# Kernel tuning notes

Measured on AMD Instinct MI355X. Metric: run time of the kernel, lower is better.

The kernel has to match this reference:

```python
import jax, jax.numpy as jnp
import numpy as np

D_MODEL = 1024
N_HEADS = 16
N_GROUPS = 4
HEAD_DIM = D_MODEL // N_HEADS
HPG = N_HEADS // N_GROUPS


def setup_inputs() -> dict:
    key = jax.random.key(0)
    ks = jax.random.split(key, 9)
    B, T = 4, 2048
    s = 1.0 / np.sqrt(D_MODEL)
    kv_dim = N_GROUPS * HEAD_DIM
    return {
        "x": jax.random.normal(ks[0], (B, T, D_MODEL), dtype=jnp.float32),
        "Wq": jax.random.normal(ks[1], (D_MODEL, D_MODEL), dtype=jnp.float32) * s,
        "bq": jnp.zeros((D_MODEL,), dtype=jnp.float32),
        "Wk": jax.random.normal(ks[2], (D_MODEL, kv_dim), dtype=jnp.float32) * s,
        "bk": jnp.zeros((kv_dim,), dtype=jnp.float32),
        "Wv": jax.random.normal(ks[3], (D_MODEL, kv_dim), dtype=jnp.float32) * s,
        "bv": jnp.zeros((kv_dim,), dtype=jnp.float32),
        "Wo": jax.random.normal(ks[4], (D_MODEL, D_MODEL), dtype=jnp.float32) * s,
        "bo": jnp.zeros((D_MODEL,), dtype=jnp.float32),
    }


def reference(x, Wq, bq, Wk, bk, Wv, bv, Wo, bo):
    B, T, _ = x.shape
    q = x @ Wq + bq                                  # [B,T,D]
    k = x @ Wk + bk                                  # [B,T,G*hd]
    v = x @ Wv + bv
    q = q.reshape(B, T, N_HEADS, HEAD_DIM).transpose(0, 2, 1, 3)   # [B,H,T,hd]
    k = k.reshape(B, T, N_GROUPS, HEAD_DIM).transpose(0, 2, 1, 3)  # [B,G,T,hd]
    v = v.reshape(B, T, N_GROUPS, HEAD_DIM).transpose(0, 2, 1, 3)
    # repeat_interleave KV groups to match Q heads
    k = jnp.repeat(k, HPG, axis=1)                   # [B,H,T,hd]
    v = jnp.repeat(v, HPG, axis=1)
    scale = 1.0 / np.sqrt(HEAD_DIM).astype(np.float32)
    scores = jnp.einsum('bhqd,bhkd->bhqk', q, k) * scale  # [B,H,T,T]
    attn = jax.nn.softmax(scores, axis=-1)
    out = jnp.einsum('bhqk,bhkd->bhqd', attn, v)     # [B,H,T,hd]
    out = out.transpose(0, 2, 1, 3).reshape(B, T, D_MODEL)
    return out @ Wo + bo
```

## Files before the change

### kernel.cpp

```cpp
#include <hip/hip_runtime.h>
#include <stdint.h>

#define D_MODEL 1024
#define T_SEQ   2048
#define BATCH   4
#define NH      16
#define NG      4
#define HD      64

#define QSCALE 0.18033688611f

typedef short bf16x8 __attribute__((ext_vector_type(8)));
typedef float f32x4  __attribute__((ext_vector_type(4)));

__device__ __forceinline__ f32x4 mfma16(bf16x8 a, bf16x8 b, f32x4 c) {
    return __builtin_amdgcn_mfma_f32_16x16x32_bf16(a, b, c, 0, 0, 0);
}

__device__ __forceinline__ unsigned short f2bf(float f) {
    __bf16 h = (__bf16)f;
    return __builtin_bit_cast(unsigned short, h);
}

__global__ __launch_bounds__(256) void prep(
        const float* __restrict__ x,  unsigned short* __restrict__ xb,
        const float* __restrict__ Wq, unsigned short* __restrict__ Wqt,
        const float* __restrict__ Wk, unsigned short* __restrict__ Wkt,
        const float* __restrict__ Wv, unsigned short* __restrict__ Wvt,
        const float* __restrict__ Wo, unsigned short* __restrict__ Wot) {
    __shared__ unsigned short sh[32][33];
    int bid = blockIdx.x;
    if (bid < 8192) {
        int i = (bid * 256 + threadIdx.x) * 4;
        float4 v = *reinterpret_cast<const float4*>(x + i);
        ushort4 o;
        o.x = f2bf(v.x); o.y = f2bf(v.y); o.z = f2bf(v.z); o.w = f2bf(v.w);
        *reinterpret_cast<ushort4*>(xb + i) = o;
        return;
    }
    bid -= 8192;
    const float* src; unsigned short* dst; int N, nbx;
    if (bid < 1024)      { src = Wq; dst = Wqt; N = 1024; nbx = 32; }
    else if (bid < 1280) { bid -= 1024; src = Wk; dst = Wkt; N = 256;  nbx = 8; }
    else if (bid < 1536) { bid -= 1280; src = Wv; dst = Wvt; N = 256;  nbx = 8; }
    else                 { bid -= 1536; src = Wo; dst = Wot; N = 1024; nbx = 32; }
    const int K = 1024;
    int n0 = (bid % nbx) * 32, k0 = (bid / nbx) * 32;
    int tx = threadIdx.x & 31, ty = threadIdx.x >> 5;
#pragma unroll
    for (int j = 0; j < 4; j++) {
        int k = ty + 8 * j;
        sh[k][tx] = f2bf(src[(size_t)(k0 + k) * N + n0 + tx]);
    }
    __syncthreads();
#pragma unroll
    for (int j = 0; j < 4; j++) {
        int n = ty + 8 * j;
        dst[(size_t)(n0 + n) * K + k0 + tx] = sh[tx][n];
    }
}

template <int MODE>
__global__ __launch_bounds__(256) void gemm128(
        const unsigned short* __restrict__ A,
        const unsigned short* __restrict__ Bt,
        const float* __restrict__ b0, const float* __restrict__ b1,
        const float* __restrict__ b2,
        void* __restrict__ Cq, void* __restrict__ Ck, void* __restrict__ Cv,
        int K) {
    __shared__ unsigned short As[128 * 64];
    __shared__ unsigned short Bs[128 * 64];

    int tid  = threadIdx.x;
    int lane = tid & 63, w = tid >> 6;
    int wr = w >> 1, wc = w & 1;

    int nx  = gridDim.x;
    int lin = blockIdx.y * nx + blockIdx.x;
    int cpx = (nx * gridDim.y) >> 3;
    int nb  = (lin & 7) * cpx + (lin >> 3);
    int m0 = (nb / nx) * 128, n0 = (nb % nx) * 128;

    int lr = lane & 15, kg = lane >> 4;

    f32x4 acc[4][4] = {};

    const unsigned short* Ab = A  + (size_t)m0 * K;
    const unsigned short* Bb = Bt + (size_t)n0 * K;

    size_t soff[4];
    unsigned short* adst[4];
    unsigned short* bdst[4];
#pragma unroll
    for (int i = 0; i < 4; i++) {
        int ci  = i * 256 + tid;
        int row = ci >> 3, ch = ci & 7;
        int csrc = ch ^ (row & 7);
        soff[i] = (size_t)row * K + csrc * 8;
        adst[i] = As + (size_t)(i * 256 + w * 64) * 8;
        bdst[i] = Bs + (size_t)(i * 256 + w * 64) * 8;
    }

    for (int kt = 0; kt < K; kt += 64) {
#pragma unroll
        for (int i = 0; i < 4; i++) {
            __builtin_amdgcn_global_load_lds(
                (const __attribute__((address_space(1))) void*)(Ab + soff[i] + kt),
                (__attribute__((address_space(3))) void*)adst[i], 16, 0, 0);
            __builtin_amdgcn_global_load_lds(
                (const __attribute__((address_space(1))) void*)(Bb + soff[i] + kt),
                (__attribute__((address_space(3))) void*)bdst[i], 16, 0, 0);
        }
        __syncthreads();

        bf16x8 af[4][2], bf[4][2];
#pragma unroll
        for (int mt = 0; mt < 4; mt++) {
            int row = wr * 64 + mt * 16 + lr;
#pragma unroll
            for (int ks = 0; ks < 2; ks++) {
                int ch = (kg + ks * 4) ^ (row & 7);
                af[mt][ks] = *reinterpret_cast<const bf16x8*>(&As[row * 64 + ch * 8]);
            }
        }
#pragma unroll
        for (int nt = 0; nt < 4; nt++) {
            int row = wc * 64 + nt * 16 + lr;
#pragma unroll
            for (int ks = 0; ks < 2; ks++) {
                int ch = (kg + ks * 4) ^ (row & 7);
                bf[nt][ks] = *reinterpret_cast<const bf16x8*>(&Bs[row * 64 + ch * 8]);
            }
        }

#pragma unroll
        for (int ks = 0; ks < 2; ks++)
#pragma unroll
            for (int mt = 0; mt < 4; mt++)
#pragma unroll
                for (int nt = 0; nt < 4; nt++)
                    acc[mt][nt] = mfma16(af[mt][ks], bf[nt][ks], acc[mt][nt]);

        __syncthreads();
    }

    int rbase = kg * 4;
#pragma unroll
    for (int nt = 0; nt < 4; nt++) {
        int col = n0 + wc * 64 + nt * 16 + lr;
        float bias;
        if (MODE == 1)            bias = b0[col];
        else if (col < 1024)      bias = b0[col];
        else if (col < 1280)      bias = b1[col - 1024];
        else                      bias = b2[col - 1280];
#pragma unroll
        for (int mt = 0; mt < 4; mt++) {
#pragma unroll
            for (int r = 0; r < 4; r++) {
                int row = m0 + wr * 64 + mt * 16 + rbase + r;
                float v = acc[mt][nt][r] + bias;
                if (MODE == 1) {
                    ((float*)Cq)[(size_t)row * 1024 + col] = v;
                } else if (col < 1024) {
                    ((unsigned short*)Cq)[(size_t)row * 1024 + col] = f2bf(v * QSCALE);
                } else if (col < 1280) {
                    int cc = col - 1024, g = cc >> 6, d = cc & 63;
                    int b = row >> 11, t = row & 2047;
                    ((unsigned short*)Ck)[(((size_t)(b * NG + g)) * T_SEQ + t) * HD + d] = f2bf(v);
                } else {
                    int cc = col - 1280, g = cc >> 6, d = cc & 63;
                    int b = row >> 11, t = row & 2047;
                    ((unsigned short*)Cv)[(((size_t)(b * NG + g)) * HD + d) * T_SEQ + t] = f2bf(v);
                }
            }
        }
    }
}

__global__ __launch_bounds__(256) void attn_fwd(
        const unsigned short* __restrict__ Q,
        const unsigned short* __restrict__ Kt,
        const unsigned short* __restrict__ Vt,
        unsigned short* __restrict__ O) {
    int tid  = threadIdx.x;
    int lane = tid & 63;
    int w    = tid >> 6;
    int qt = blockIdx.x, h = blockIdx.y, b = blockIdx.z;
    int g = h >> 2;
    int lr  = lane & 15;
    int grp = lane >> 4;
    int ko  = grp * 8;
    int q0  = qt * 128 + w * 32;

    __shared__ unsigned short Kl[2][64 * 64];
    __shared__ unsigned short Vl[2][64 * 64];

    const unsigned short* Kp = Kt + ((size_t)(b * NG + g)) * T_SEQ * HD;
    const unsigned short* Vp = Vt + ((size_t)(b * NG + g)) * HD * T_SEQ;

    bf16x8 qf[2][2];
#pragma unroll
    for (int qi = 0; qi < 2; qi++) {
        const unsigned short* Qp =
            Q + ((size_t)(b * T_SEQ + q0 + qi * 16 + lr)) * D_MODEL + h * HD;
        qf[qi][0] = *reinterpret_cast<const bf16x8*>(Qp + ko);
        qf[qi][1] = *reinterpret_cast<const bf16x8*>(Qp + 32 + ko);
    }

    f32x4 oacc[2][4] = {};
    f32x4 den[2] = {};
    bf16x8 ones;
#pragma unroll
    for (int j = 0; j < 8; j++) ones[j] = (short)0x3F80;

    int loff[4][2];
#pragma unroll
    for (int c = 0; c < 4; c++) {
        int row = c * 16 + lr;
#pragma unroll
        for (int s = 0; s < 2; s++)
            loff[c][s] = row * 64 + (((s * 4 + grp) ^ (row & 7)) * 8);
    }

    const unsigned short* gkb[2];
    const unsigned short* gvb[2];
    unsigned short* lkd[2];
#pragma unroll
    for (int i = 0; i < 2; i++) {
        int ci  = i * 256 + tid;
        int row = ci >> 3, ch = ci & 7;
        int csrc = ch ^ (row & 7);
        int kp = 32 * (row >> 5) + 4 * ((row >> 4) & 1)
               + 8 * ((row >> 2) & 3) + (row & 3);
        gkb[i] = Kp + (size_t)kp * HD + csrc * 8;
        gvb[i] = Vp + (size_t)row * T_SEQ + csrc * 8;
        lkd[i] = (unsigned short*)((size_t)(i * 256 + w * 64) * 8);
    }

    auto STAGE = [&](int buf, int j0) {
#pragma unroll
        for (int i = 0; i < 2; i++) {
            size_t ldoff = (size_t)lkd[i];
            __builtin_amdgcn_global_load_lds(
                (const __attribute__((address_space(1))) void*)(gkb[i] + ((size_t)j0 << 6)),
                (__attribute__((address_space(3))) void*)(&Kl[buf][0] + ldoff), 16, 0, 0);
            __builtin_amdgcn_global_load_lds(
                (const __attribute__((address_space(1))) void*)(gvb[i] + j0),
                (__attribute__((address_space(3))) void*)(&Vl[buf][0] + ldoff), 16, 0, 0);
        }
    };

    auto do_tile = [&](int cur, int jt) {
        if (jt + 1 < T_SEQ / 64) STAGE(cur ^ 1, (jt + 1) * 64);

        const unsigned short* kb = &Kl[cur][0];
        const unsigned short* vb = &Vl[cur][0];

        bf16x8 kf[4][2], vf[4][2];
#pragma unroll
        for (int t = 0; t < 4; t++)
#pragma unroll
            for (int ks = 0; ks < 2; ks++)
                kf[t][ks] = *reinterpret_cast<const bf16x8*>(kb + loff[t][ks]);
#pragma unroll
        for (int dt = 0; dt < 4; dt++)
#pragma unroll
            for (int kh = 0; kh < 2; kh++)
                vf[dt][kh] = *reinterpret_cast<const bf16x8*>(vb + loff[dt][kh]);

#pragma unroll
        for (int qi = 0; qi < 2; qi++) {
            f32x4 s[4];
            __builtin_amdgcn_s_setprio(1);
#pragma unroll
            for (int t = 0; t < 4; t++) {
                f32x4 a = {};
                a = mfma16(kf[t][0], qf[qi][0], a);
                a = mfma16(kf[t][1], qf[qi][1], a);
                s[t] = a;
            }
            __builtin_amdgcn_s_setprio(0);

            float p[4][4];
#pragma unroll
            for (int t = 0; t < 4; t++)
#pragma unroll
                for (int r = 0; r < 4; r++)
                    asm("v_exp_f32 %0, %1" : "=v"(p[t][r]) : "v"(s[t][r]));

            bf16x8 pf0, pf1;
#pragma unroll
            for (int j = 0; j < 4; j++) {
                pf0[j]     = (short)f2bf(p[0][j]);
                pf0[j + 4] = (short)f2bf(p[1][j]);
                pf1[j]     = (short)f2bf(p[2][j]);
                pf1[j + 4] = (short)f2bf(p[3][j]);
            }

            __builtin_amdgcn_s_setprio(1);
#pragma unroll
            for (int dt = 0; dt < 4; dt++) {
                oacc[qi][dt] = mfma16(vf[dt][0], pf0, oacc[qi][dt]);
                oacc[qi][dt] = mfma16(vf[dt][1], pf1, oacc[qi][dt]);
            }
            den[qi] = mfma16(ones, pf0, den[qi]);
            den[qi] = mfma16(ones, pf1, den[qi]);
            __builtin_amdgcn_s_setprio(0);
        }

        asm volatile("s_waitcnt vmcnt(0)" ::: "memory");
        __syncthreads();
    };

    STAGE(0, 0);
    asm volatile("s_waitcnt vmcnt(0)" ::: "memory");
    __syncthreads();

    for (int jt = 0; jt < T_SEQ / 64; jt += 2) {
        do_tile(0, jt);
        do_tile(1, jt + 1);
    }

#pragma unroll
    for (int qi = 0; qi < 2; qi++) {
        float rinv = 1.0f / den[qi][0];
        size_t rowbase = ((size_t)(b * T_SEQ + q0 + qi * 16 + lr)) * D_MODEL + h * HD;
#pragma unroll
        for (int dt = 0; dt < 4; dt++) {
            ushort4 o;
#pragma unroll
            for (int r = 0; r < 4; r++)
                ((unsigned short*)&o)[r] = f2bf(oacc[qi][dt][r] * rinv);
            *reinterpret_cast<ushort4*>(&O[rowbase + dt * 16 + 4 * grp]) = o;
        }
    }
}

extern "C" void kernel_launch(void* const* d_in, const int* in_sizes, int n_in,
                              void* d_out, int out_size, void* d_ws, size_t ws_size,
                              hipStream_t stream) {
    const float* x  = (const float*)d_in[0];
    const float* Wq = (const float*)d_in[1];
    const float* bq = (const float*)d_in[2];
    const float* Wk = (const float*)d_in[3];
    const float* bk = (const float*)d_in[4];
    const float* Wv = (const float*)d_in[5];
    const float* bv = (const float*)d_in[6];
    const float* Wo = (const float*)d_in[7];
    const float* bo = (const float*)d_in[8];

    char* ws = (char*)d_ws;
    unsigned short* xb  = (unsigned short*)(ws);
    unsigned short* Wqt = (unsigned short*)(ws + 16777216);
    unsigned short* Wkt = (unsigned short*)(ws + 18874368);
    unsigned short* Wvt = (unsigned short*)(ws + 19398656);
    unsigned short* Wot = (unsigned short*)(ws + 19922944);
    unsigned short* Qb  = (unsigned short*)(ws + 22020096);
    unsigned short* Kb  = (unsigned short*)(ws + 38797312);
    unsigned short* Vtb = (unsigned short*)(ws + 42991616);

    prep<<<dim3(8192 + 2560), 256, 0, stream>>>(
        x, xb, Wq, Wqt, Wk, Wkt, Wv, Wvt, Wo, Wot);

    gemm128<0><<<dim3(12, 64), 256, 0, stream>>>(
        xb, Wqt, bq, bk, bv, Qb, Kb, Vtb, 1024);

    attn_fwd<<<dim3(T_SEQ / 128, NH, BATCH), 256, 0, stream>>>(Qb, Kb, Vtb, xb);

    gemm128<1><<<dim3(8, 64), 256, 0, stream>>>(
        xb, Wot, bo, nullptr, nullptr, d_out, nullptr, nullptr, 1024);
}
```

Baseline: 162.4 us.

## Triple-buffer K/V tiles in attention with two-ahead prefetch and partial vmcnt waits

Moves the attention kernel's K/V staging from double to triple buffering in LDS, so loads are issued two tiles ahead. Each step now waits only until the older tile's loads have completed (vmcnt(4)) and uses a raw s_barrier, so global_load_lds transfers can stay in flight across the barrier. This costs 50% more LDS per block, which may reduce occupancy, and depends on exact vmcnt accounting for correctness.

```diff
diff --git a/kernel.cpp b/kernel.cpp
--- a/kernel.cpp
+++ b/kernel.cpp
@@ -192,8 +192,8 @@
     int ko  = grp * 8;
     int q0  = qt * 128 + w * 32;
 
-    __shared__ unsigned short Kl[2][64 * 64];
-    __shared__ unsigned short Vl[2][64 * 64];
+    __shared__ unsigned short Kl[3][64 * 64];
+    __shared__ unsigned short Vl[3][64 * 64];
 
     const unsigned short* Kp = Kt + ((size_t)(b * NG + g)) * T_SEQ * HD;
     const unsigned short* Vp = Vt + ((size_t)(b * NG + g)) * HD * T_SEQ;
@@ -224,7 +224,7 @@
 
     const unsigned short* gkb[2];
     const unsigned short* gvb[2];
-    unsigned short* lkd[2];
+    size_t lkd[2];
 #pragma unroll
     for (int i = 0; i < 2; i++) {
         int ci  = i * 256 + tid;
@@ -234,25 +234,22 @@
                + 8 * ((row >> 2) & 3) + (row & 3);
         gkb[i] = Kp + (size_t)kp * HD + csrc * 8;
         gvb[i] = Vp + (size_t)row * T_SEQ + csrc * 8;
-        lkd[i] = (unsigned short*)((size_t)(i * 256 + w * 64) * 8);
+        lkd[i] = (size_t)(i * 256 + w * 64) * 8;
     }
 
     auto STAGE = [&](int buf, int j0) {
 #pragma unroll
         for (int i = 0; i < 2; i++) {
-            size_t ldoff = (size_t)lkd[i];
             __builtin_amdgcn_global_load_lds(
                 (const __attribute__((address_space(1))) void*)(gkb[i] + ((size_t)j0 << 6)),
-                (__attribute__((address_space(3))) void*)(&Kl[buf][0] + ldoff), 16, 0, 0);
+                (__attribute__((address_space(3))) void*)(&Kl[buf][0] + lkd[i]), 16, 0, 0);
             __builtin_amdgcn_global_load_lds(
                 (const __attribute__((address_space(1))) void*)(gvb[i] + j0),
-                (__attribute__((address_space(3))) void*)(&Vl[buf][0] + ldoff), 16, 0, 0);
+                (__attribute__((address_space(3))) void*)(&Vl[buf][0] + lkd[i]), 16, 0, 0);
         }
     };
 
-    auto do_tile = [&](int cur, int jt) {
-        if (jt + 1 < T_SEQ / 64) STAGE(cur ^ 1, (jt + 1) * 64);
-
+    auto COMPUTE = [&](int cur) {
         const unsigned short* kb = &Kl[cur][0];
         const unsigned short* vb = &Vl[cur][0];
 
@@ -307,19 +304,35 @@
             den[qi] = mfma16(ones, pf1, den[qi]);
             __builtin_amdgcn_s_setprio(0);
         }
-
+    };
+
+    auto do_tile = [&](int cur, int jt) {
+        STAGE((cur + 2) % 3, (jt + 2) * 64);
+        COMPUTE(cur);
+        asm volatile("s_waitcnt vmcnt(4)" ::: "memory");
+        __builtin_amdgcn_s_barrier();
+        asm volatile("" ::: "memory");
+    };
+    auto do_tail = [&](int cur) {
+        COMPUTE(cur);
         asm volatile("s_waitcnt vmcnt(0)" ::: "memory");
-        __syncthreads();
+        __builtin_amdgcn_s_barrier();
+        asm volatile("" ::: "memory");
     };
 
     STAGE(0, 0);
-    asm volatile("s_waitcnt vmcnt(0)" ::: "memory");
-    __syncthreads();
-
-    for (int jt = 0; jt < T_SEQ / 64; jt += 2) {
+    STAGE(1, 64);
+    asm volatile("s_waitcnt vmcnt(4)" ::: "memory");
+    __builtin_amdgcn_s_barrier();
+    asm volatile("" ::: "memory");
+
+    for (int jt = 0; jt < 30; jt += 3) {
         do_tile(0, jt);
         do_tile(1, jt + 1);
-    }
+        do_tile(2, jt + 2);
+    }
+    do_tail(0);
+    do_tail(1);
 
 #pragma unroll
     for (int qi = 0; qi < 2; qi++) {
```

Result: no change. 161.6 us (-0.5%).
